# Kernel tuning notes

Hardware: AMD Instinct MI355X
Metric: run time of the kernel (lower is better)

## Reference

```python
import jax, jax.numpy as jnp
import numpy as np

B, C, H, W = 8, 64, 64, 64


def _conv1x1(x, Wm, b):
    # 1x1 conv == per-pixel channel matmul: (O,C) x (B,C,H,W) -> (B,O,H,W)
    return jnp.einsum('oc,bchw->bohw', Wm, x) + b[:, None, None]


def setup_inputs() -> dict:
    key = jax.random.key(0)
    ks = jax.random.split(key, 9)
    s = 1.0 / np.sqrt(C)  # torch Conv2d default init scale
    return {
        'x': jax.random.normal(ks[0], (B, C, H, W), dtype=jnp.float32),
        'Wq': jax.random.normal(ks[1], (C, C), dtype=jnp.float32) * s,
        'bq': jax.random.normal(ks[2], (C,), dtype=jnp.float32) * s,
        'Wk': jax.random.normal(ks[3], (C, C), dtype=jnp.float32) * s,
        'bk': jax.random.normal(ks[4], (C,), dtype=jnp.float32) * s,
        'Wv': jax.random.normal(ks[5], (C, C), dtype=jnp.float32) * s,
        'bv': jax.random.normal(ks[6], (C,), dtype=jnp.float32) * s,
        'Wo': jax.random.normal(ks[7], (C, C), dtype=jnp.float32) * s,
        'bo': jax.random.normal(ks[8], (C,), dtype=jnp.float32) * s,
    }


def reference(x, Wq, bq, Wk, bk, Wv, bv, Wo, bo):
    b_, c_, h_, w_ = x.shape
    n = h_ * w_
    q = _conv1x1(x, Wq, bq).reshape(b_, c_, n)  # (B,C,N)
    k = _conv1x1(x, Wk, bk).reshape(b_, c_, n)
    v = _conv1x1(x, Wv, bv).reshape(b_, c_, n)
    # scores = q^T k  (no 1/sqrt(d) scaling, per original)
    scores = jnp.einsum('bci,bcj->bij', q, k)          # (B,N,N)
    attn = jax.nn.softmax(scores, axis=-1)
    # res = bmm(v, attn): res[b,c,i] = sum_j v[b,c,j] * attn[b,j,i] (swapped order)
    res = jnp.einsum('bcj,bji->bci', v, attn).reshape(b_, c_, h_, w_)
    return _conv1x1(res, Wo, bo) + res
```

## Files before the change

kernel.cpp:

```cpp
#include <hip/hip_runtime.h>
#include <stdint.h>

#define NPIX 4096
#define LOG2E 1.44269504088896340736f

typedef __bf16 bf16x8 __attribute__((ext_vector_type(8)));
typedef float  f32x4  __attribute__((ext_vector_type(4)));
typedef unsigned long long ull;

union FragU {
  bf16x8 f;
  uint4  u;
  ull    q[2];
  unsigned short s[8];
};

static __device__ __forceinline__ unsigned short f2bf(float x) {
  unsigned int u = __float_as_uint(x);
  u += 0x7FFFu + ((u >> 16) & 1u);
  return (unsigned short)(u >> 16);
}
static __device__ __forceinline__ float bf2f(unsigned short s) {
  return __uint_as_float(((unsigned int)s) << 16);
}
static __device__ __forceinline__ unsigned int pack2(unsigned short a, unsigned short b) {
  return (unsigned int)a | ((unsigned int)b << 16);
}
static __device__ __forceinline__ float e2(float x) { return __builtin_amdgcn_exp2f(x); }

static __device__ __forceinline__ bf16x8 load_frag(const unsigned short* base, int byteOff) {
  const char* p = reinterpret_cast<const char*>(base) + byteOff;
  uint2 a = *reinterpret_cast<const uint2*>(p);
  uint2 b = *reinterpret_cast<const uint2*>(p + 32);
  FragU fu;
  fu.u = make_uint4(a.x, a.y, b.x, b.y);
  return fu.f;
}

static __device__ __forceinline__ int rotc(int row, int col) {
  return (col + ((row & 7) << 4)) & 127;
}

static __device__ __forceinline__ bf16x8 lds_frag(const char* base, int row, int cb) {
  const int rb = row << 7;
  ull a = *reinterpret_cast<const ull*>(base + rb + rotc(row, cb));
  ull b = *reinterpret_cast<const ull*>(base + rb + rotc(row, cb + 32));
  FragU fu;
  fu.q[0] = a; fu.q[1] = b;
  return fu.f;
}

static __device__ __forceinline__ void stage_write(char* dst, int t, uint4 r0, uint4 r1) {
  const int o0 = t * 16;
  const int o1 = 4096 + t * 16;
  const int w0 = o0 >> 7, w1 = o1 >> 7;
  *reinterpret_cast<uint4*>(dst + (w0 << 7) + rotc(w0, o0 & 127)) = r0;
  *reinterpret_cast<uint4*>(dst + (w1 << 7) + rotc(w1, o1 & 127)) = r1;
}

__global__ __launch_bounds__(256) void qkv_proj(
    const float* __restrict__ x,
    const float* __restrict__ Wq, const float* __restrict__ bq,
    const float* __restrict__ Wk, const float* __restrict__ bk,
    const float* __restrict__ Wv, const float* __restrict__ bv,
    unsigned short* __restrict__ qT, unsigned short* __restrict__ kT,
    unsigned short* __restrict__ vC)
{
  const int t  = threadIdx.x;
  const int b  = blockIdx.y;
  const int n  = blockIdx.x * 256 + t;
  const int o0 = blockIdx.z * 16;

  float xv[64];
  #pragma unroll
  for (int c = 0; c < 64; ++c) xv[c] = x[((size_t)b * 64 + c) * NPIX + n];

  const float* Wp[3] = {Wq, Wk, Wv};
  const float* Bp[3] = {bq, bk, bv};

  #pragma unroll
  for (int p = 0; p < 3; ++p) {
    const float* W  = Wp[p];
    const float* Bv = Bp[p];
    unsigned short outv[16];
    #pragma unroll
    for (int oo = 0; oo < 16; ++oo) {
      float acc = Bv[o0 + oo];
      #pragma unroll
      for (int c = 0; c < 64; ++c) acc += W[(o0 + oo) * 64 + c] * xv[c];
      if (p == 0) acc *= LOG2E;
      outv[oo] = f2bf(acc);
    }
    if (p < 2) {
      unsigned short* dst = (p == 0 ? qT : kT) + ((size_t)b * NPIX + n) * 64 + o0;
      uint4 w0 = make_uint4(pack2(outv[0], outv[1]),  pack2(outv[2], outv[3]),
                            pack2(outv[4], outv[5]),  pack2(outv[6], outv[7]));
      uint4 w1 = make_uint4(pack2(outv[8], outv[9]),  pack2(outv[10], outv[11]),
                            pack2(outv[12], outv[13]), pack2(outv[14], outv[15]));
      *reinterpret_cast<uint4*>(dst)     = w0;
      *reinterpret_cast<uint4*>(dst + 8) = w1;
    } else {
      #pragma unroll
      for (int oo = 0; oo < 16; ++oo)
        vC[((size_t)b * 64 + o0 + oo) * NPIX + n] = outv[oo];
    }
  }
}

__global__ __launch_bounds__(256, 2) void attn_rowsum(
    const unsigned short* __restrict__ qT, const unsigned short* __restrict__ kT,
    float* __restrict__ Zpart, int ntiles)
{
  __shared__ __align__(16) char sK[2 * 8192];

  const int t    = threadIdx.x;
  const int b    = blockIdx.y;
  const int part = blockIdx.z;
  const int lane = t & 63;
  const int wv   = t >> 6;
  const int j0   = blockIdx.x * 256 + wv * 64;
  const int lr   = lane & 15;
  const int lg   = lane >> 4;

  bf16x8 aq0[4], aq1[4];
  #pragma unroll
  for (int f = 0; f < 4; ++f) {
    const unsigned short* qrow = qT + ((size_t)b * NPIX + j0 + f * 16 + lr) * 64;
    aq0[f] = load_frag(qrow, lg * 8);
    aq1[f] = load_frag(qrow, 64 + lg * 8);
  }

  const char* kbase = reinterpret_cast<const char*>(kT) + (size_t)b * NPIX * 128
                      + (size_t)part * ntiles * 8192;

  float zacc[4][4];
  #pragma unroll
  for (int f = 0; f < 4; ++f)
    #pragma unroll
    for (int r = 0; r < 4; ++r) zacc[f][r] = 0.f;

  uint4 r0 = *reinterpret_cast<const uint4*>(kbase + t * 16);
  uint4 r1 = *reinterpret_cast<const uint4*>(kbase + 4096 + t * 16);

  for (int tile = 0; tile < ntiles; ++tile) {
    char* buf = sK + (tile & 1) * 8192;
    stage_write(buf, t, r0, r1);
    __syncthreads();
    if (tile + 1 < ntiles) {
      const char* src = kbase + (size_t)(tile + 1) * 8192;
      r0 = *reinterpret_cast<const uint4*>(src + t * 16);
      r1 = *reinterpret_cast<const uint4*>(src + 4096 + t * 16);
    }
    bf16x8 kf0[4], kf1[4];
    #pragma unroll
    for (int s = 0; s < 4; ++s) {
      kf0[s] = lds_frag(buf, s * 16 + lr, lg * 8);
      kf1[s] = lds_frag(buf, s * 16 + lr, 64 + lg * 8);
    }
    #pragma unroll
    for (int f = 0; f < 4; ++f) {
      #pragma unroll
      for (int s = 0; s < 4; ++s) {
        f32x4 S = {0.f, 0.f, 0.f, 0.f};
        S = __builtin_amdgcn_mfma_f32_16x16x32_bf16(aq0[f], kf0[s], S, 0, 0, 0);
        S = __builtin_amdgcn_mfma_f32_16x16x32_bf16(aq1[f], kf1[s], S, 0, 0, 0);
        zacc[f][0] += e2(S[0]);
        zacc[f][1] += e2(S[1]);
        zacc[f][2] += e2(S[2]);
        zacc[f][3] += e2(S[3]);
      }
    }
    __syncthreads();
  }

  #pragma unroll
  for (int f = 0; f < 4; ++f) {
    #pragma unroll
    for (int m = 8; m >= 1; m >>= 1) {
      #pragma unroll
      for (int r = 0; r < 4; ++r) zacc[f][r] += __shfl_xor(zacc[f][r], m, 64);
    }
  }
  if (lr == 0) {
    float* dst = Zpart + ((size_t)part * 8 + b) * NPIX + j0 + lg * 4;
    #pragma unroll
    for (int f = 0; f < 4; ++f) {
      #pragma unroll
      for (int r = 0; r < 4; ++r) dst[f * 16 + r] = zacc[f][r];
    }
  }
}

__global__ __launch_bounds__(256) void vscale(
    unsigned short* __restrict__ vC, const float* __restrict__ Zpart, int nparts)
{
  const int idx = blockIdx.x * 256 + threadIdx.x;
  const int jc  = idx & 511;
  const int b   = idx >> 15;
  unsigned short* p = vC + (size_t)idx * 8;
  const float* zb = Zpart + (size_t)b * NPIX + jc * 8;
  float z[8];
  #pragma unroll
  for (int e = 0; e < 8; ++e) z[e] = 0.f;
  for (int pp = 0; pp < nparts; ++pp) {
    const float* zp = zb + (size_t)pp * 8 * NPIX;
    #pragma unroll
    for (int e = 0; e < 8; ++e) z[e] += zp[e];
  }
  FragU v;
  v.q[0] = reinterpret_cast<const ull*>(p)[0];
  v.q[1] = reinterpret_cast<const ull*>(p)[1];
  #pragma unroll
  for (int e = 0; e < 8; ++e) v.s[e] = f2bf(bf2f(v.s[e]) * (1.0f / z[e]));
  reinterpret_cast<ull*>(p)[0] = v.q[0];
  reinterpret_cast<ull*>(p)[1] = v.q[1];
}

__global__ __launch_bounds__(256, 2) void attn_pv(
    const unsigned short* __restrict__ qT, const unsigned short* __restrict__ kT,
    const unsigned short* __restrict__ vC, float* __restrict__ resP, int ntiles)
{
  __shared__ __align__(16) char sQ[2 * 8192];
  __shared__ __align__(16) char sV[2 * 8192];

  const int t    = threadIdx.x;
  const int b    = blockIdx.y;
  const int part = blockIdx.z;
  const int lane = t & 63;
  const int wv   = t >> 6;
  const int i0   = blockIdx.x * 256 + wv * 64;
  const int lr   = lane & 15;
  const int lg   = lane >> 4;
  const int jstart = part * ntiles * 64;

  bf16x8 kf0[4], kf1[4];
  #pragma unroll
  for (int s = 0; s < 4; ++s) {
    const unsigned short* krow = kT + ((size_t)b * NPIX + i0 + s * 16 + lr) * 64;
    kf0[s] = load_frag(krow, lg * 8);
    kf1[s] = load_frag(krow, 64 + lg * 8);
  }

  const char* qbase = reinterpret_cast<const char*>(qT) + ((size_t)b * NPIX + jstart) * 128;
  const char* vbase = reinterpret_cast<const char*>(vC) + (size_t)b * 64 * 8192
                      + (size_t)jstart * 2;

  const int vo0_row = (t * 16) >> 7,        vo0_col = (t * 16) & 127;
  const int vo1_row = (4096 + t * 16) >> 7, vo1_col = (4096 + t * 16) & 127;

  f32x4 acc[4][4];
  #pragma unroll
  for (int m = 0; m < 4; ++m)
    #pragma unroll
    for (int s = 0; s < 4; ++s) acc[m][s] = (f32x4){0.f, 0.f, 0.f, 0.f};

  uint4 q0 = *reinterpret_cast<const uint4*>(qbase + t * 16);
  uint4 q1 = *reinterpret_cast<const uint4*>(qbase + 4096 + t * 16);
  uint4 v0 = *reinterpret_cast<const uint4*>(vbase + (size_t)vo0_row * 8192 + vo0_col);
  uint4 v1 = *reinterpret_cast<const uint4*>(vbase + (size_t)vo1_row * 8192 + vo1_col);

  for (int tile = 0; tile < ntiles; ++tile) {
    char* Qt = sQ + (tile & 1) * 8192;
    char* Vt = sV + (tile & 1) * 8192;
    stage_write(Qt, t, q0, q1);
    stage_write(Vt, t, v0, v1);
    __syncthreads();
    if (tile + 1 < ntiles) {
      const char* qsrc = qbase + (size_t)(tile + 1) * 8192;
      q0 = *reinterpret_cast<const uint4*>(qsrc + t * 16);
      q1 = *reinterpret_cast<const uint4*>(qsrc + 4096 + t * 16);
      const int jb = (tile + 1) * 128;
      v0 = *reinterpret_cast<const uint4*>(vbase + (size_t)vo0_row * 8192 + jb + vo0_col);
      v1 = *reinterpret_cast<const uint4*>(vbase + (size_t)vo1_row * 8192 + jb + vo1_col);
    }

    bf16x8 qf0[4], qf1[4], vf0[4], vf1[4];
    #pragma unroll
    for (int f = 0; f < 4; ++f) {
      qf0[f] = lds_frag(Qt, f * 16 + lr, lg * 8);
      qf1[f] = lds_frag(Qt, f * 16 + lr, 64 + lg * 8);
    }
    #pragma unroll
    for (int m = 0; m < 4; ++m) {
      vf0[m] = lds_frag(Vt, m * 16 + lr, lg * 8);
      vf1[m] = lds_frag(Vt, m * 16 + lr, 64 + lg * 8);
    }

    #pragma unroll
    for (int s = 0; s < 4; ++s) {
      f32x4 sj[4];
      #pragma unroll
      for (int f = 0; f < 4; ++f) {
        sj[f] = (f32x4){0.f, 0.f, 0.f, 0.f};
        sj[f] = __builtin_amdgcn_mfma_f32_16x16x32_bf16(qf0[f], kf0[s], sj[f], 0, 0, 0);
        sj[f] = __builtin_amdgcn_mfma_f32_16x16x32_bf16(qf1[f], kf1[s], sj[f], 0, 0, 0);
      }
      FragU pe0, pe1;
      #pragma unroll
      for (int r = 0; r < 4; ++r) {
        pe0.f[r]     = (__bf16)e2(sj[0][r]);
        pe0.f[4 + r] = (__bf16)e2(sj[1][r]);
        pe1.f[r]     = (__bf16)e2(sj[2][r]);
        pe1.f[4 + r] = (__bf16)e2(sj[3][r]);
      }
      #pragma unroll
      for (int m = 0; m < 4; ++m) {
        acc[m][s] = __builtin_amdgcn_mfma_f32_16x16x32_bf16(vf0[m], pe0.f, acc[m][s], 0, 0, 0);
        acc[m][s] = __builtin_amdgcn_mfma_f32_16x16x32_bf16(vf1[m], pe1.f, acc[m][s], 0, 0, 0);
      }
    }
    __syncthreads();
  }

  float* rbase = resP + ((size_t)part * 8 + b) * 64 * NPIX;
  #pragma unroll
  for (int m = 0; m < 4; ++m) {
    #pragma unroll
    for (int s = 0; s < 4; ++s) {
      #pragma unroll
      for (int r = 0; r < 4; ++r) {
        rbase[(size_t)(m * 16 + lg * 4 + r) * NPIX + i0 + s * 16 + lr] = acc[m][s][r];
      }
    }
  }
}

__global__ __launch_bounds__(256) void resred(
    const float* __restrict__ resP, float* __restrict__ res, int nparts)
{
  const size_t idx = (size_t)blockIdx.x * 256 + threadIdx.x;
  const float4* src = reinterpret_cast<const float4*>(resP) + idx;
  float4 a = src[0];
  for (int p = 1; p < nparts; ++p) {
    float4 b = src[(size_t)p * 524288];
    a.x += b.x; a.y += b.y; a.z += b.z; a.w += b.w;
  }
  reinterpret_cast<float4*>(res)[idx] = a;
}

__global__ __launch_bounds__(256) void out_proj(
    const float* __restrict__ res, const float* __restrict__ Wo,
    const float* __restrict__ bo, float* __restrict__ out)
{
  const int t  = threadIdx.x;
  const int b  = blockIdx.y;
  const int n  = blockIdx.x * 256 + t;
  const int o0 = blockIdx.z * 16;

  float rv[64];
  #pragma unroll
  for (int c = 0; c < 64; ++c) rv[c] = res[((size_t)b * 64 + c) * NPIX + n];

  #pragma unroll
  for (int oo = 0; oo < 16; ++oo) {
    float acc = bo[o0 + oo];
    #pragma unroll
    for (int c = 0; c < 64; ++c) acc += Wo[(o0 + oo) * 64 + c] * rv[c];
    acc += res[((size_t)b * 64 + o0 + oo) * NPIX + n];
    out[((size_t)b * 64 + o0 + oo) * NPIX + n] = acc;
  }
}

extern "C" void kernel_launch(void* const* d_in, const int* in_sizes, int n_in,
                              void* d_out, int out_size, void* d_ws, size_t ws_size,
                              hipStream_t stream) {
  const float* x  = (const float*)d_in[0];
  const float* Wq = (const float*)d_in[1];
  const float* bq = (const float*)d_in[2];
  const float* Wk = (const float*)d_in[3];
  const float* bk = (const float*)d_in[4];
  const float* Wv = (const float*)d_in[5];
  const float* bv = (const float*)d_in[6];
  const float* Wo = (const float*)d_in[7];
  const float* bo = (const float*)d_in[8];
  float* out = (float*)d_out;

  char* ws = (char*)d_ws;
  unsigned short* qT = (unsigned short*)(ws);
  unsigned short* kT = (unsigned short*)(ws + ((size_t)4 << 20));
  float* res         = (float*)(ws);
  unsigned short* vC = (unsigned short*)(ws + ((size_t)8 << 20));
  float* Zpart       = (float*)(ws + ((size_t)12 << 20));
  float* resP        = (float*)(ws + ((size_t)13 << 20));

  int nparts;
  const size_t MB = (size_t)1 << 20;
  if      (ws_size >= 13 * MB + 8 * 8 * MB) nparts = 8;
  else if (ws_size >= 13 * MB + 4 * 8 * MB) nparts = 4;
  else if (ws_size >= 13 * MB + 2 * 8 * MB) nparts = 2;
  else                                      nparts = 1;
  const int ntiles = 64 / nparts;

  qkv_proj<<<dim3(16, 8, 4), 256, 0, stream>>>(x, Wq, bq, Wk, bk, Wv, bv, qT, kT, vC);
  attn_rowsum<<<dim3(16, 8, nparts), 256, 0, stream>>>(qT, kT, Zpart, ntiles);
  vscale<<<dim3(1024), 256, 0, stream>>>(vC, Zpart, nparts);
  attn_pv<<<dim3(16, 8, nparts), 256, 0, stream>>>(qT, kT, vC, resP, ntiles);
  resred<<<dim3(2048), 256, 0, stream>>>(resP, res, nparts);
  out_proj<<<dim3(16, 8, 4), 256, 0, stream>>>(res, Wo, bo, out);
}
```

Baseline: 216.4 us.

## Store attention partials in bf16 and change LDS swizzle to XOR-permuted 8-byte slots

The per-split partial results written by the attention kernel are now stored as bf16 instead of fp32, halving partial-buffer traffic and the reduction kernel's reads. The workspace thresholds shrink to match, so more splits may be chosen for a given workspace. The LDS layout swizzle is also changed to a permutation of 8-byte slots with an XOR on the upper row bit, aimed at reducing bank conflicts. Rounding partials to bf16 adds precision loss in the summed attention output.

```diff
diff --git a/kernel.cpp b/kernel.cpp
--- a/kernel.cpp
+++ b/kernel.cpp
@@ -37,25 +37,28 @@
   return fu.f;
 }
 
-static __device__ __forceinline__ int rotc(int row, int col) {
-  return (col + ((row & 7) << 4)) & 127;
+static __device__ __forceinline__ int pib(int row, int beta) {
+  return ((beta + 2 * (row & 7)) & 15) ^ ((row >> 3) & 1);
 }
 
 static __device__ __forceinline__ bf16x8 lds_frag(const char* base, int row, int cb) {
   const int rb = row << 7;
-  ull a = *reinterpret_cast<const ull*>(base + rb + rotc(row, cb));
-  ull b = *reinterpret_cast<const ull*>(base + rb + rotc(row, cb + 32));
+  ull a = *reinterpret_cast<const ull*>(base + rb + (pib(row, cb >> 3) << 3));
+  ull b = *reinterpret_cast<const ull*>(base + rb + (pib(row, (cb + 32) >> 3) << 3));
   FragU fu;
   fu.q[0] = a; fu.q[1] = b;
   return fu.f;
 }
 
 static __device__ __forceinline__ void stage_write(char* dst, int t, uint4 r0, uint4 r1) {
-  const int o0 = t * 16;
-  const int o1 = 4096 + t * 16;
+  const int o0 = t * 16, o1 = 4096 + t * 16;
   const int w0 = o0 >> 7, w1 = o1 >> 7;
-  *reinterpret_cast<uint4*>(dst + (w0 << 7) + rotc(w0, o0 & 127)) = r0;
-  *reinterpret_cast<uint4*>(dst + (w1 << 7) + rotc(w1, o1 & 127)) = r1;
+  const int e0 = ((((o0 & 127) >> 3) + 2 * (w0 & 7)) & 15);
+  const int e1 = ((((o1 & 127) >> 3) + 2 * (w1 & 7)) & 15);
+  const uint4 a0 = ((w0 >> 3) & 1) ? make_uint4(r0.z, r0.w, r0.x, r0.y) : r0;
+  const uint4 a1 = ((w1 >> 3) & 1) ? make_uint4(r1.z, r1.w, r1.x, r1.y) : r1;
+  *reinterpret_cast<uint4*>(dst + (w0 << 7) + (e0 << 3)) = a0;
+  *reinterpret_cast<uint4*>(dst + (w1 << 7) + (e1 << 3)) = a1;
 }
 
 __global__ __launch_bounds__(256) void qkv_proj(
@@ -218,7 +221,8 @@
 
 __global__ __launch_bounds__(256, 2) void attn_pv(
     const unsigned short* __restrict__ qT, const unsigned short* __restrict__ kT,
-    const unsigned short* __restrict__ vC, float* __restrict__ resP, int ntiles)
+    const unsigned short* __restrict__ vC, unsigned short* __restrict__ resP,
+    int ntiles)
 {
   __shared__ __align__(16) char sQ[2 * 8192];
   __shared__ __align__(16) char sV[2 * 8192];
@@ -312,30 +316,37 @@
     __syncthreads();
   }
 
-  float* rbase = resP + ((size_t)part * 8 + b) * 64 * NPIX;
+  unsigned short* rbase = resP + ((size_t)part * 8 + b) * 64 * NPIX;
   #pragma unroll
   for (int m = 0; m < 4; ++m) {
     #pragma unroll
     for (int s = 0; s < 4; ++s) {
       #pragma unroll
       for (int r = 0; r < 4; ++r) {
-        rbase[(size_t)(m * 16 + lg * 4 + r) * NPIX + i0 + s * 16 + lr] = acc[m][s][r];
+        rbase[(size_t)(m * 16 + lg * 4 + r) * NPIX + i0 + s * 16 + lr] = f2bf(acc[m][s][r]);
       }
     }
   }
 }
 
 __global__ __launch_bounds__(256) void resred(
-    const float* __restrict__ resP, float* __restrict__ res, int nparts)
+    const unsigned short* __restrict__ resP, float* __restrict__ res, int nparts)
 {
   const size_t idx = (size_t)blockIdx.x * 256 + threadIdx.x;
-  const float4* src = reinterpret_cast<const float4*>(resP) + idx;
-  float4 a = src[0];
-  for (int p = 1; p < nparts; ++p) {
-    float4 b = src[(size_t)p * 524288];
-    a.x += b.x; a.y += b.y; a.z += b.z; a.w += b.w;
-  }
-  reinterpret_cast<float4*>(res)[idx] = a;
+  const uint4* src = reinterpret_cast<const uint4*>(resP) + idx;
+  float a[8];
+  #pragma unroll
+  for (int e = 0; e < 8; ++e) a[e] = 0.f;
+  for (int p = 0; p < nparts; ++p) {
+    FragU u;
+    u.u = src[(size_t)p * 262144];
+    #pragma unroll
+    for (int e = 0; e < 8; ++e) a[e] += bf2f(u.s[e]);
+  }
+  float4 o0 = make_float4(a[0], a[1], a[2], a[3]);
+  float4 o1 = make_float4(a[4], a[5], a[6], a[7]);
+  reinterpret_cast<float4*>(res)[idx * 2]     = o0;
+  reinterpret_cast<float4*>(res)[idx * 2 + 1] = o1;
 }
 
 __global__ __launch_bounds__(256) void out_proj(
@@ -376,18 +387,18 @@
   float* out = (float*)d_out;
 
   char* ws = (char*)d_ws;
-  unsigned short* qT = (unsigned short*)(ws);
-  unsigned short* kT = (unsigned short*)(ws + ((size_t)4 << 20));
-  float* res         = (float*)(ws);
-  unsigned short* vC = (unsigned short*)(ws + ((size_t)8 << 20));
-  float* Zpart       = (float*)(ws + ((size_t)12 << 20));
-  float* resP        = (float*)(ws + ((size_t)13 << 20));
+  unsigned short* qT   = (unsigned short*)(ws);
+  unsigned short* kT   = (unsigned short*)(ws + ((size_t)4 << 20));
+  float* res           = (float*)(ws);
+  unsigned short* vC   = (unsigned short*)(ws + ((size_t)8 << 20));
+  float* Zpart         = (float*)(ws + ((size_t)12 << 20));
+  unsigned short* resP = (unsigned short*)(ws + ((size_t)13 << 20));
 
   int nparts;
   const size_t MB = (size_t)1 << 20;
-  if      (ws_size >= 13 * MB + 8 * 8 * MB) nparts = 8;
-  else if (ws_size >= 13 * MB + 4 * 8 * MB) nparts = 4;
-  else if (ws_size >= 13 * MB + 2 * 8 * MB) nparts = 2;
+  if      (ws_size >= 13 * MB + 8 * 4 * MB) nparts = 8;
+  else if (ws_size >= 13 * MB + 4 * 4 * MB) nparts = 4;
+  else if (ws_size >= 13 * MB + 2 * 4 * MB) nparts = 2;
   else                                      nparts = 1;
   const int ntiles = 64 / nparts;
 
@@ -395,6 +406,6 @@
   attn_rowsum<<<dim3(16, 8, nparts), 256, 0, stream>>>(qT, kT, Zpart, ntiles);
   vscale<<<dim3(1024), 256, 0, stream>>>(vC, Zpart, nparts);
   attn_pv<<<dim3(16, 8, nparts), 256, 0, stream>>>(qT, kT, vC, resP, ntiles);
-  resred<<<dim3(2048), 256, 0, stream>>>(resP, res, nparts);
+  resred<<<dim3(1024), 256, 0, stream>>>(resP, res, nparts);
   out_proj<<<dim3(16, 8, 4), 256, 0, stream>>>(res, Wo, bo, out);
 }
```

Measured after the change: 213.9 us. Within noise of the previous version (-1.2%).
